# Performance work log

Measured on AMD Instinct MI355X. Metric: run time of the kernel, lower is better.

Reference implementation:

```python
import jax, jax.numpy as jnp
import numpy as np

B, T, C = 2, 2048, 2048
H, KV, D = 16, 4, 128   # n_head, n_kv_head, head_dim
EPS = 1.1920929e-07     # torch.finfo(float32).eps, F.rms_norm default


def setup_inputs() -> dict:
    key = jax.random.key(0)
    ks = jax.random.split(key, 7)
    x = jax.random.normal(ks[0], (B, T, C), dtype=jnp.float32)
    # rope angles: cos/sin of positions, broadcastable to [B,T,H,D//2]
    inv_freq = 1.0 / (10000.0 ** (jnp.arange(0, D // 2, dtype=jnp.float32) / (D // 2)))
    ang = jnp.arange(T, dtype=jnp.float32)[:, None] * inv_freq[None, :]
    cos = jnp.cos(ang)[None, :, None, :]  # [1,T,1,D/2]
    sin = jnp.sin(ang)[None, :, None, :]
    s = 0.02
    Wq = jax.random.normal(ks[1], (C, H * D), dtype=jnp.float32) * s
    Wk = jax.random.normal(ks[2], (C, KV * D), dtype=jnp.float32) * s
    Wv = jax.random.normal(ks[3], (C, KV * D), dtype=jnp.float32) * s
    Wo = jax.random.normal(ks[4], (C, C), dtype=jnp.float32) * s
    return {"x": x, "cos": cos, "sin": sin, "Wq": Wq, "Wk": Wk, "Wv": Wv, "Wo": Wo}


def _rope(t, cos, sin):
    d = t.shape[-1] // 2
    t1, t2 = t[..., :d], t[..., d:]
    return jnp.concatenate([t1 * cos + t2 * sin, -t1 * sin + t2 * cos], axis=-1)


def _rmsnorm(t):
    return t * jax.lax.rsqrt(jnp.mean(t * t, axis=-1, keepdims=True) + EPS)


def reference(x, cos, sin, Wq, Wk, Wv, Wo):
    q = (x @ Wq).reshape(B, T, H, D)
    k = (x @ Wk).reshape(B, T, KV, D)
    v = (x @ Wv).reshape(B, T, KV, D)
    q = _rmsnorm(_rope(q, cos, sin))
    k = _rmsnorm(_rope(k, cos, sin))
    # [B, KV, G, T, D] query grouped per kv head (GQA)
    G = H // KV
    qh = q.transpose(0, 2, 1, 3).reshape(B, KV, G, T, D)
    kh = k.transpose(0, 2, 1, 3)  # [B, KV, T, D]
    vh = v.transpose(0, 2, 1, 3)
    scale = 1.0 / np.sqrt(D).astype(np.float32)
    scores = jnp.einsum('bhgqd,bhkd->bhgqk', qh, kh) * scale
    causal = jnp.tril(jnp.ones((T, T), dtype=bool))
    scores = jnp.where(causal, scores, jnp.finfo(scores.dtype).min)
    attn = jax.nn.softmax(scores, axis=-1)
    y = jnp.einsum('bhgqk,bhkd->bhgqd', attn, vh)  # [B,KV,G,T,D]
    y = y.reshape(B, H, T, D).transpose(0, 2, 1, 3).reshape(B, T, C)
    return y @ Wo
```

## Files before the change

kernel.cpp:

```cpp
#include <hip/hip_runtime.h>

using bf16x8 = __attribute__((ext_vector_type(8))) short;
using f32x4  = __attribute__((ext_vector_type(4))) float;

#define B_  2
#define T_  2048
#define C_  2048
#define H_  16
#define KV_ 4
#define D_  128

__device__ __forceinline__ unsigned short f2b(float f) {
  union { float f; unsigned int u; } v; v.f = f;
  unsigned int r = v.u + 0x7fffu + ((v.u >> 16) & 1u);
  return (unsigned short)(r >> 16);
}
__device__ __forceinline__ float b2f(unsigned short u) {
  union { unsigned int u; float f; } v; v.u = ((unsigned int)u) << 16;
  return v.f;
}
__device__ __forceinline__ void gld_lds16(const void* g, void* l) {
  __builtin_amdgcn_global_load_lds(
      (__attribute__((address_space(1))) void*)g,
      (__attribute__((address_space(3))) void*)l, 16, 0, 0);
}

__global__ void cast_bf16_k(const float* __restrict__ in, unsigned short* __restrict__ out) {
  int i = blockIdx.x * 256 + threadIdx.x;
  float4 f = ((const float4*)in)[i];
  ushort4 u; u.x = f2b(f.x); u.y = f2b(f.y); u.z = f2b(f.z); u.w = f2b(f.w);
  ((ushort4*)out)[i] = u;
}

__global__ void wtrans(const float* __restrict__ W, unsigned short* __restrict__ Wt,
                       int K, int N) {
  __shared__ float s[32][33];
  int n0 = blockIdx.x * 32, k0 = blockIdx.y * 32;
  int tx = threadIdx.x, ty = threadIdx.y;
  #pragma unroll
  for (int yy = 0; yy < 32; yy += 8)
    s[ty + yy][tx] = W[(size_t)(k0 + ty + yy) * N + n0 + tx];
  __syncthreads();
  #pragma unroll
  for (int yy = 0; yy < 32; yy += 8)
    Wt[(size_t)(n0 + ty + yy) * K + k0 + tx] = f2b(s[tx][ty + yy]);
}

template <bool OUT_BF16>
__device__ __forceinline__ void gemm_tile(
    const unsigned short* __restrict__ A, const unsigned short* __restrict__ Bt,
    void* __restrict__ Cv, int K, int ldc, int m0, int n0b, int n0c,
    unsigned short* sA, unsigned short* sB)
{
  const int tid  = threadIdx.x;
  const int lane = tid & 63, w = tid >> 6;
  const int quad = lane >> 4, l16 = lane & 15;
  const int wm = (w >> 1) * 64, wn = (w & 1) * 64;

  f32x4 acc[4][4] = {};

  const unsigned short* Abase = A  + (size_t)m0  * K;
  const unsigned short* Bbase = Bt + (size_t)n0b * K;

  for (int k0 = 0; k0 < K; k0 += 32) {
    #pragma unroll
    for (int r = 0; r < 2; ++r) {
      int c = tid + r * 256;
      int row = c >> 2, col = (c & 3) * 8;
      gld_lds16(Abase + (size_t)row * K + k0 + col, sA + c * 8);
      gld_lds16(Bbase + (size_t)row * K + k0 + col, sB + c * 8);
    }
    __syncthreads();
    bf16x8 af[4], bfr[4];
    #pragma unroll
    for (int i = 0; i < 4; ++i)
      af[i]  = *(const bf16x8*)(sA + (wm + i * 16 + l16) * 32 + quad * 8);
    #pragma unroll
    for (int j = 0; j < 4; ++j)
      bfr[j] = *(const bf16x8*)(sB + (wn + j * 16 + l16) * 32 + quad * 8);
    #pragma unroll
    for (int i = 0; i < 4; ++i)
      #pragma unroll
      for (int j = 0; j < 4; ++j)
        acc[i][j] = __builtin_amdgcn_mfma_f32_16x16x32_bf16(af[i], bfr[j], acc[i][j], 0, 0, 0);
    __syncthreads();
  }
  #pragma unroll
  for (int i = 0; i < 4; ++i) {
    #pragma unroll
    for (int r = 0; r < 4; ++r) {
      int row = m0 + wm + i * 16 + quad * 4 + r;
      #pragma unroll
      for (int j = 0; j < 4; ++j) {
        int col = n0c + wn + j * 16 + l16;
        float v = acc[i][j][r];
        if (OUT_BF16) ((unsigned short*)Cv)[(size_t)row * ldc + col] = f2b(v);
        else          ((float*)Cv)[(size_t)row * ldc + col] = v;
      }
    }
  }
}

__global__ void qkv_gemm(const unsigned short* __restrict__ xb,
                         const unsigned short* __restrict__ Wqt,
                         const unsigned short* __restrict__ Wkt,
                         const unsigned short* __restrict__ Wvt,
                         unsigned short* q, unsigned short* k, unsigned short* v) {
  __shared__ unsigned short sA[128 * 32], sB[128 * 32];
  int nt = blockIdx.x, mt = blockIdx.y;
  const unsigned short* Bt; unsigned short* C; int n0, ldc;
  if (nt < 16)      { Bt = Wqt; C = q; n0 = nt * 128;        ldc = H_ * D_;  }
  else if (nt < 20) { Bt = Wkt; C = k; n0 = (nt - 16) * 128; ldc = KV_ * D_; }
  else              { Bt = Wvt; C = v; n0 = (nt - 20) * 128; ldc = KV_ * D_; }
  gemm_tile<true>(xb, Bt, C, C_, ldc, mt * 128, n0, n0, sA, sB);
}

__global__ void out_gemm(const unsigned short* __restrict__ yb,
                         const unsigned short* __restrict__ Wot,
                         float* __restrict__ out) {
  __shared__ unsigned short sA[128 * 32], sB[128 * 32];
  gemm_tile<false>(yb, Wot, out, C_, C_, blockIdx.y * 128, blockIdx.x * 128, blockIdx.x * 128,
                   sA, sB);
}

template <int NH>
__global__ void ropenorm(const unsigned short* __restrict__ in,
                         const float* __restrict__ cs, const float* __restrict__ sn,
                         unsigned short* __restrict__ out, float oscale) {
  int row  = blockIdx.x * 4 + (threadIdx.x >> 6);
  int lane = threadIdx.x & 63;
  int head = row % NH;
  int t = (row / NH) & (T_ - 1);
  int b = row / (NH * T_);
  const unsigned short* p = in + (size_t)row * D_;
  float t1 = b2f(p[lane]), t2 = b2f(p[lane + 64]);
  float c = cs[t * 64 + lane], s = sn[t * 64 + lane];
  float o1 = t1 * c + t2 * s;
  float o2 = t2 * c - t1 * s;
  float ss = o1 * o1 + o2 * o2;
  #pragma unroll
  for (int off = 32; off > 0; off >>= 1) ss += __shfl_xor(ss, off, 64);
  float r = rsqrtf(ss * (1.0f / 128.0f) + 1.1920929e-07f) * oscale;
  size_t base = ((size_t)((b * NH + head) * 128 + (t >> 4))) * 2048 + (size_t)(t & 15) * 8;
  out[base + (size_t)(lane >> 3) * 128 + (lane & 7)]       = f2b(o1 * r);
  out[base + (size_t)(8 + (lane >> 3)) * 128 + (lane & 7)] = f2b(o2 * r);
}

__global__ void vfrag_k(const unsigned short* __restrict__ v, unsigned short* __restrict__ vf) {
  int it = blockIdx.x;
  int b = blockIdx.y >> 2, kv = blockIdx.y & 3;
  int d = threadIdx.x, ty = threadIdx.y;
  int t0 = it * 64;
  size_t obase = ((size_t)((b * KV_ + kv) * 32 + it)) * 8192
               + (size_t)(d >> 4) * 1024 + (size_t)(d & 15) * 8;
  #pragma unroll
  for (int tcg = 0; tcg < 4; ++tcg) {
    int tc = ty * 4 + tcg;
    unsigned short val[8];
    #pragma unroll
    for (int e = 0; e < 8; ++e)
      val[e] = v[(((size_t)(b * T_) + t0 + tc * 8 + e) * KV_ + kv) * D_ + d];
    ushort4 u0 = {val[0], val[1], val[2], val[3]};
    ushort4 u1 = {val[4], val[5], val[6], val[7]};
    *(ushort4*)(vf + obase + (size_t)tc * 128)     = u0;
    *(ushort4*)(vf + obase + (size_t)tc * 128 + 4) = u1;
  }
}

__global__ __launch_bounds__(256, 2) void attn_kernel(
    const unsigned short* __restrict__ qf, const unsigned short* __restrict__ kf,
    const unsigned short* __restrict__ vf, unsigned short* __restrict__ yb) {
  __shared__ unsigned short sP[4 * 32 * 72];

  const int xp = (int)blockIdx.x;
  const int b = xp >> 2, kv = xp & 3;
  const int yp = (int)blockIdx.y;
  const int j = yp >> 1, hh = yp & 1;
  const int tid = threadIdx.x;
  const int w = tid >> 6, lane = tid & 63;
  const int quad = lane >> 4, l16 = lane & 15;
  const int qt = (w & 1) ? (63 - j) : j;
  const int h = kv * 4 + hh * 2 + (w >> 1);
  const int q0 = qt * 32;
  const int ntile = (qt >> 1) + 1;
  unsigned short* myP = sP + w * (32 * 72);

  const unsigned short* Qf = qf + ((size_t)(b * H_ + h) * 128 + qt * 2) * 2048;
  const unsigned short* Kf = kf + (size_t)(b * KV_ + kv) * 128 * 2048;
  const unsigned short* Vf = vf + (size_t)(b * KV_ + kv) * 32 * 8192;

  bf16x8 bq[2][4];
  #pragma unroll
  for (int i = 0; i < 2; ++i)
    #pragma unroll
    for (int kk = 0; kk < 4; ++kk)
      bq[i][kk] = *(const bf16x8*)(Qf + (size_t)i * 2048 + (kk * 4 + quad) * 128 + l16 * 8);

  float l_i[2] = {0.f, 0.f};
  f32x4 o[2][8] = {};

  for (int it = 0; it < ntile; ++it) {
    const int t0 = it * 64;
    const unsigned short* Kt = Kf + (size_t)(it * 4) * 2048;
    const unsigned short* Vt = Vf + (size_t)it * 8192;

    f32x4 sc[4][2] = {};
    #pragma unroll
    for (int kk = 0; kk < 4; ++kk) {
      bf16x8 ak[4];
      #pragma unroll
      for (int jt = 0; jt < 4; ++jt)
        ak[jt] = *(const bf16x8*)(Kt + (size_t)jt * 2048 + (kk * 4 + quad) * 128 + l16 * 8);
      #pragma unroll
      for (int jt = 0; jt < 4; ++jt)
        #pragma unroll
        for (int i = 0; i < 2; ++i)
          sc[jt][i] = __builtin_amdgcn_mfma_f32_16x16x32_bf16(ak[jt], bq[i][kk], sc[jt][i], 0, 0, 0);
    }

    bf16x8 bv[2][8];
    #pragma unroll
    for (int kk2 = 0; kk2 < 2; ++kk2)
      #pragma unroll
      for (int jj = 0; jj < 8; ++jj)
        bv[kk2][jj] = *(const bf16x8*)(Vt + (size_t)jj * 1024 + (kk2 * 4 + quad) * 128 + l16 * 8);

    if (it == ntile - 1) {
      #pragma unroll
      for (int jt = 0; jt < 4; ++jt) {
        int kg = t0 + jt * 16 + quad * 4;
        #pragma unroll
        for (int i = 0; i < 2; ++i) {
          int qg = q0 + i * 16 + l16;
          #pragma unroll
          for (int r = 0; r < 4; ++r)
            if (kg + r > qg) sc[jt][i][r] = -3.0e38f;
        }
      }
    }

    #pragma unroll
    for (int i = 0; i < 2; ++i) {
      float part = 0.f;
      #pragma unroll
      for (int jt = 0; jt < 4; ++jt)
        #pragma unroll
        for (int r = 0; r < 4; ++r) {
          float p = __expf(sc[jt][i][r] - 12.0f);
          sc[jt][i][r] = p; part += p;
        }
      l_i[i] += part;
    }

    #pragma unroll
    for (int i = 0; i < 2; ++i)
      #pragma unroll
      for (int jt = 0; jt < 4; ++jt) {
        ushort4 u;
        u.x = f2b(sc[jt][i][0]); u.y = f2b(sc[jt][i][1]);
        u.z = f2b(sc[jt][i][2]); u.w = f2b(sc[jt][i][3]);
        *(ushort4*)(myP + (i * 16 + l16) * 72 + jt * 16 + quad * 4) = u;
      }

    #pragma unroll
    for (int kk2 = 0; kk2 < 2; ++kk2) {
      bf16x8 ap[2];
      #pragma unroll
      for (int i = 0; i < 2; ++i)
        ap[i] = *(const bf16x8*)(myP + (i * 16 + l16) * 72 + kk2 * 32 + quad * 8);
      #pragma unroll
      for (int i = 0; i < 2; ++i)
        #pragma unroll
        for (int jj = 0; jj < 8; ++jj)
          o[i][jj] = __builtin_amdgcn_mfma_f32_16x16x32_bf16(ap[i], bv[kk2][jj], o[i][jj], 0, 0, 0);
    }
  }

  #pragma unroll
  for (int i = 0; i < 2; ++i) {
    float l = l_i[i];
    l += __shfl_xor(l, 16, 64);
    l += __shfl_xor(l, 32, 64);
    float linv = 1.0f / l;
    float lr[4];
    #pragma unroll
    for (int r = 0; r < 4; ++r) lr[r] = __shfl(linv, quad * 4 + r, 64);
    #pragma unroll
    for (int r = 0; r < 4; ++r) {
      int tg = q0 + i * 16 + quad * 4 + r;
      unsigned short* yr = yb + (((size_t)(b * T_ + tg)) * H_ + h) * D_;
      #pragma unroll
      for (int jj = 0; jj < 8; ++jj)
        yr[jj * 16 + l16] = f2b(o[i][jj][r] * lr[r]);
    }
  }
}

extern "C" void kernel_launch(void* const* d_in, const int* in_sizes, int n_in,
                              void* d_out, int out_size, void* d_ws, size_t ws_size,
                              hipStream_t stream) {
  (void)in_sizes; (void)n_in; (void)out_size; (void)ws_size;
  const float* x  = (const float*)d_in[0];
  const float* cs = (const float*)d_in[1];
  const float* sn = (const float*)d_in[2];
  const float* Wq = (const float*)d_in[3];
  const float* Wk = (const float*)d_in[4];
  const float* Wv = (const float*)d_in[5];
  const float* Wo = (const float*)d_in[6];
  float* out = (float*)d_out;
  char* ws = (char*)d_ws;

  unsigned short* xb   = (unsigned short*)(ws + 0);
  unsigned short* Wqt  = (unsigned short*)(ws + 16777216);
  unsigned short* Wkt  = (unsigned short*)(ws + 25165824);
  unsigned short* Wvt  = (unsigned short*)(ws + 27262976);
  unsigned short* Wot  = (unsigned short*)(ws + 29360128);
  unsigned short* qraw = (unsigned short*)(ws + 37748736);
  unsigned short* kraw = (unsigned short*)(ws + 54525952);
  unsigned short* vraw = (unsigned short*)(ws + 58720256);
  unsigned short* qfr  = (unsigned short*)(ws + 62914560);
  unsigned short* kfr  = (unsigned short*)(ws + 79691776);
  unsigned short* vfr  = (unsigned short*)(ws + 83886080);
  unsigned short* yb   = qraw;

  cast_bf16_k<<<dim3(8192), dim3(256), 0, stream>>>(x, xb);
  wtrans<<<dim3(64, 64), dim3(32, 8), 0, stream>>>(Wq, Wqt, 2048, 2048);
  wtrans<<<dim3(16, 64), dim3(32, 8), 0, stream>>>(Wk, Wkt, 2048, 512);
  wtrans<<<dim3(16, 64), dim3(32, 8), 0, stream>>>(Wv, Wvt, 2048, 512);
  wtrans<<<dim3(64, 64), dim3(32, 8), 0, stream>>>(Wo, Wot, 2048, 2048);
  qkv_gemm<<<dim3(24, 32), dim3(256), 0, stream>>>(xb, Wqt, Wkt, Wvt, qraw, kraw, vraw);
  ropenorm<16><<<dim3(16384), dim3(256), 0, stream>>>(qraw, cs, sn, qfr, 0.08838834764831845f);
  ropenorm<4><<<dim3(4096),  dim3(256), 0, stream>>>(kraw, cs, sn, kfr, 1.0f);
  vfrag_k<<<dim3(32, 8), dim3(128, 2), 0, stream>>>(vraw, vfr);
  attn_kernel<<<dim3(8, 64), dim3(256), 0, stream>>>(qfr, kfr, vfr, yb);
  out_gemm<<<dim3(16, 32), dim3(256), 0, stream>>>(yb, Wot, out);
}
```

Measured before the change: 332.7 us.

## Split attention KV loop across two wave pairs and reduce partials via LDS

Each block now handles one head, and its two wave halves take alternating KV tiles; the halves then combine their partial outputs and row sums through shared memory before normalizing. The grid doubles and launch bounds rise to 4 blocks per CU, aiming at more parallelism and occupancy along the causal KV dimension. The float-to-bf16 packing of P also switches to the hardware packed-convert instruction. The cost is an extra LDS reduction with two block barriers, about 34KB of shared memory, and tighter register limits.

```diff
diff --git a/kernel.cpp b/kernel.cpp
--- a/kernel.cpp
+++ b/kernel.cpp
@@ -18,6 +18,11 @@
 __device__ __forceinline__ float b2f(unsigned short u) {
   union { unsigned int u; float f; } v; v.u = ((unsigned int)u) << 16;
   return v.f;
+}
+__device__ __forceinline__ unsigned int cvt_pk_bf16(float lo, float hi) {
+  unsigned int r;
+  asm("v_cvt_pk_bf16_f32 %0, %1, %2" : "=v"(r) : "v"(lo), "v"(hi));
+  return r;
 }
 __device__ __forceinline__ void gld_lds16(const void* g, void* l) {
   __builtin_amdgcn_global_load_lds(
@@ -167,23 +172,24 @@
   }
 }
 
-__global__ __launch_bounds__(256, 2) void attn_kernel(
+__global__ __launch_bounds__(256, 4) void attn_kernel(
     const unsigned short* __restrict__ qf, const unsigned short* __restrict__ kf,
     const unsigned short* __restrict__ vf, unsigned short* __restrict__ yb) {
-  __shared__ unsigned short sP[4 * 32 * 72];
+  __shared__ __align__(16) char smem[34048];
 
   const int xp = (int)blockIdx.x;
   const int b = xp >> 2, kv = xp & 3;
   const int yp = (int)blockIdx.y;
-  const int j = yp >> 1, hh = yp & 1;
+  const int j = yp >> 2, hp = yp & 3;
   const int tid = threadIdx.x;
   const int w = tid >> 6, lane = tid & 63;
   const int quad = lane >> 4, l16 = lane & 15;
-  const int qt = (w & 1) ? (63 - j) : j;
-  const int h = kv * 4 + hh * 2 + (w >> 1);
+  const int qsel = w & 1, half = w >> 1;
+  const int qt = qsel ? (63 - j) : j;
+  const int h = kv * 4 + hp;
   const int q0 = qt * 32;
   const int ntile = (qt >> 1) + 1;
-  unsigned short* myP = sP + w * (32 * 72);
+  unsigned short* myP = (unsigned short*)smem + w * (32 * 72);
 
   const unsigned short* Qf = qf + ((size_t)(b * H_ + h) * 128 + qt * 2) * 2048;
   const unsigned short* Kf = kf + (size_t)(b * KV_ + kv) * 128 * 2048;
@@ -199,7 +205,7 @@
   float l_i[2] = {0.f, 0.f};
   f32x4 o[2][8] = {};
 
-  for (int it = 0; it < ntile; ++it) {
+  for (int it = half; it < ntile; it += 2) {
     const int t0 = it * 64;
     const unsigned short* Kt = Kf + (size_t)(it * 4) * 2048;
     const unsigned short* Vt = Vf + (size_t)it * 8192;
@@ -256,10 +262,10 @@
     for (int i = 0; i < 2; ++i)
       #pragma unroll
       for (int jt = 0; jt < 4; ++jt) {
-        ushort4 u;
-        u.x = f2b(sc[jt][i][0]); u.y = f2b(sc[jt][i][1]);
-        u.z = f2b(sc[jt][i][2]); u.w = f2b(sc[jt][i][3]);
-        *(ushort4*)(myP + (i * 16 + l16) * 72 + jt * 16 + quad * 4) = u;
+        uint2 uu;
+        uu.x = cvt_pk_bf16(sc[jt][i][0], sc[jt][i][1]);
+        uu.y = cvt_pk_bf16(sc[jt][i][2], sc[jt][i][3]);
+        *(uint2*)(myP + (i * 16 + l16) * 72 + jt * 16 + quad * 4) = uu;
       }
 
     #pragma unroll
@@ -276,22 +282,48 @@
     }
   }
 
+  float lsum[2];
   #pragma unroll
   for (int i = 0; i < 2; ++i) {
     float l = l_i[i];
     l += __shfl_xor(l, 16, 64);
     l += __shfl_xor(l, 32, 64);
-    float linv = 1.0f / l;
-    float lr[4];
-    #pragma unroll
-    for (int r = 0; r < 4; ++r) lr[r] = __shfl(linv, quad * 4 + r, 64);
-    #pragma unroll
-    for (int r = 0; r < 4; ++r) {
-      int tg = q0 + i * 16 + quad * 4 + r;
-      unsigned short* yr = yb + (((size_t)(b * T_ + tg)) * H_ + h) * D_;
+    lsum[i] = l;
+  }
+
+  __syncthreads();
+  float* oc = (float*)smem + qsel * (32 * 132);
+  float* lc = (float*)smem + 2 * (32 * 132) + qsel * 32;
+  if (half == 1) {
+    #pragma unroll
+    for (int i = 0; i < 2; ++i) {
+      if (quad == 0) lc[i * 16 + l16] = lsum[i];
       #pragma unroll
       for (int jj = 0; jj < 8; ++jj)
-        yr[jj * 16 + l16] = f2b(o[i][jj][r] * lr[r]);
+        #pragma unroll
+        for (int r = 0; r < 4; ++r)
+          oc[(i * 16 + quad * 4 + r) * 132 + jj * 16 + l16] = o[i][jj][r];
+    }
+  }
+  __syncthreads();
+  if (half == 0) {
+    #pragma unroll
+    for (int i = 0; i < 2; ++i) {
+      float l = lsum[i] + lc[i * 16 + l16];
+      float linv = 1.0f / l;
+      float lr[4];
+      #pragma unroll
+      for (int r = 0; r < 4; ++r) lr[r] = __shfl(linv, quad * 4 + r, 64);
+      #pragma unroll
+      for (int r = 0; r < 4; ++r) {
+        int tg = q0 + i * 16 + quad * 4 + r;
+        unsigned short* yr = yb + (((size_t)(b * T_ + tg)) * H_ + h) * D_;
+        #pragma unroll
+        for (int jj = 0; jj < 8; ++jj) {
+          float vsum = o[i][jj][r] + oc[(i * 16 + quad * 4 + r) * 132 + jj * 16 + l16];
+          yr[jj * 16 + l16] = f2b(vsum * lr[r]);
+        }
+      }
     }
   }
 }
@@ -332,6 +364,6 @@
   ropenorm<16><<<dim3(16384), dim3(256), 0, stream>>>(qraw, cs, sn, qfr, 0.08838834764831845f);
   ropenorm<4><<<dim3(4096),  dim3(256), 0, stream>>>(kraw, cs, sn, kfr, 1.0f);
   vfrag_k<<<dim3(32, 8), dim3(128, 2), 0, stream>>>(vraw, vfr);
-  attn_kernel<<<dim3(8, 64), dim3(256), 0, stream>>>(qfr, kfr, vfr, yb);
+  attn_kernel<<<dim3(8, 128), dim3(256), 0, stream>>>(qfr, kfr, vfr, yb);
   out_gemm<<<dim3(16, 32), dim3(256), 0, stream>>>(yb, Wot, out);
 }
```

Result: slower. 487.6 us (+46.6%).
